# Kernel optimization log

Measured on AMD Instinct MI355X. Metric: run time of the kernel, lower is better.

Reference implementation:

```python
import jax, jax.numpy as jnp
import numpy as np

D_MODEL = 1024
NUM_HEADS = 16
D_K = D_MODEL // NUM_HEADS


def setup_inputs() -> dict:
    key = jax.random.key(0)
    ks = jax.random.split(key, 9)
    B, S = 2, 2048
    s_in = 1.0 / np.sqrt(D_MODEL)
    x = jax.random.normal(ks[0], (B, S, D_MODEL), dtype=jnp.float32)
    # Linear weights stored as (in_features, out_features): y = x @ W + b
    Wq = jax.random.uniform(ks[1], (D_MODEL, D_MODEL), jnp.float32, -s_in, s_in)
    bq = jax.random.uniform(ks[2], (D_MODEL,), jnp.float32, -s_in, s_in)
    Wk = jax.random.uniform(ks[3], (D_MODEL, D_K), jnp.float32, -s_in, s_in)
    bk = jax.random.uniform(ks[4], (D_K,), jnp.float32, -s_in, s_in)
    Wv = jax.random.uniform(ks[5], (D_MODEL, D_K), jnp.float32, -s_in, s_in)
    bv = jax.random.uniform(ks[6], (D_K,), jnp.float32, -s_in, s_in)
    Wo = jax.random.uniform(ks[7], (D_MODEL, D_MODEL), jnp.float32, -s_in, s_in)
    bo = jax.random.uniform(ks[8], (D_MODEL,), jnp.float32, -s_in, s_in)
    return {"x": x, "Wq": Wq, "bq": bq, "Wk": Wk, "bk": bk,
            "Wv": Wv, "bv": bv, "Wo": Wo, "bo": bo}


def reference(x, Wq, bq, Wk, bk, Wv, bv, Wo, bo):
    B, S, _ = x.shape
    H, Dk = NUM_HEADS, D_K
    # Projections
    Q = (x @ Wq + bq).reshape(B, S, H, Dk).transpose(0, 2, 1, 3)  # [B,H,S,Dk]
    K = x @ Wk + bk                                               # [B,S,Dk] single KV head
    V = x @ Wv + bv                                               # [B,S,Dk]
    # Scores: query heads broadcast against the single shared KV head
    scores = jnp.einsum('bhqd,bkd->bhqk', Q, K) / jnp.sqrt(jnp.float32(Dk))
    attn = jax.nn.softmax(scores, axis=-1)                        # [B,H,S,S]
    out = jnp.einsum('bhqk,bkd->bhqd', attn, V)                   # [B,H,S,Dk]
    out = out.transpose(0, 2, 1, 3).reshape(B, S, H * Dk)         # [B,S,d_model]
    return out @ Wo + bo
```

## Files before the change

### kernel.cpp

```cpp
#include <hip/hip_runtime.h>
#include <hip/hip_bf16.h>

typedef __attribute__((ext_vector_type(8))) short bf16x8;
typedef __attribute__((ext_vector_type(4))) float f32x4;
typedef __attribute__((ext_vector_type(16))) float f32x16;
typedef __attribute__((ext_vector_type(4))) unsigned short ushort4v;

#define QSCALE 0.1803368801111204f

__device__ __forceinline__ unsigned short f2bf(float f) {
  union { float f; unsigned int u; } x; x.f = f;
  unsigned int u = x.u;
  unsigned int r = (u + 0x7fffu + ((u >> 16) & 1u)) >> 16;
  return (unsigned short)r;
}

__device__ __forceinline__ void gll16(const unsigned short* g, unsigned short* l) {
  __builtin_amdgcn_global_load_lds(
      (const __attribute__((address_space(1))) unsigned int*)g,
      (__attribute__((address_space(3))) unsigned int*)l, 16, 0, 0);
}

__global__ __launch_bounds__(256) void prep_kernel(
    const float* __restrict__ x,
    const float* __restrict__ Wq, const float* __restrict__ Wk,
    const float* __restrict__ Wv, const float* __restrict__ Wo,
    unsigned short* __restrict__ xb,
    unsigned short* __restrict__ QKVt, unsigned short* __restrict__ Wot) {
  int z = blockIdx.z;
  if (z == 4) {
    size_t base = ((size_t)(blockIdx.y * 32 + blockIdx.x)) * 4096 + threadIdx.x * 16;
#pragma unroll
    for (int c = 0; c < 4; ++c) {
      float4 v = *(const float4*)(x + base + c * 4);
      ushort4v o = { f2bf(v.x), f2bf(v.y), f2bf(v.z), f2bf(v.w) };
      *(ushort4v*)(xb + base + c * 4) = o;
    }
    return;
  }
  __shared__ float t[32][33];
  const float* src;
  unsigned short* dst;
  int C, rowoff;
  if (z == 0)      { src = Wq; dst = QKVt; C = 1024; rowoff = 0; }
  else if (z == 1) { src = Wk; dst = QKVt; C = 64;   rowoff = 1024; }
  else if (z == 2) { src = Wv; dst = QKVt; C = 64;   rowoff = 1088; }
  else             { src = Wo; dst = Wot;  C = 1024; rowoff = 0; }
  int c0 = blockIdx.x * 32, r0 = blockIdx.y * 32;
  if (c0 >= C) return;
  int tx = threadIdx.x & 31, ty = threadIdx.x >> 5;
#pragma unroll
  for (int i = 0; i < 32; i += 8)
    t[ty + i][tx] = src[(size_t)(r0 + ty + i) * C + c0 + tx];
  __syncthreads();
#pragma unroll
  for (int i = 0; i < 32; i += 8)
    dst[(size_t)(rowoff + c0 + ty + i) * 1024 + r0 + tx] = f2bf(t[tx][ty + i]);
}

template <typename OutT, bool QKVMODE>
__global__ __launch_bounds__(512, 2) void gemm_bf16_kernel(
    const unsigned short* __restrict__ A, const unsigned short* __restrict__ Bt,
    const float* __restrict__ b0, const float* __restrict__ b1,
    const float* __restrict__ b2, OutT* __restrict__ C,
    unsigned short* __restrict__ Vt, int M, int N, int K) {
  __shared__ __align__(16) unsigned short As[2][128 * 32];
  __shared__ __align__(16) unsigned short Bs[2][64 * 32];
  int tid = threadIdx.x;
  int wid = tid >> 6, lane = tid & 63;
  int l15 = lane & 15, quad = lane >> 4;
  int m0 = blockIdx.x * 128, n0 = blockIdx.y * 64;
  int mw = (wid >> 1) * 32, nw = (wid & 1) * 32;
  f32x4 acc[2][2];
#pragma unroll
  for (int i = 0; i < 2; i++)
#pragma unroll
    for (int j = 0; j < 2; j++)
#pragma unroll
      for (int e = 0; e < 4; ++e) acc[i][j][e] = 0.f;

  bool isA = (wid < 4);
  int u = tid & 255;
  int srow = u >> 2;
  int gq = (u & 3) ^ ((srow >> 1) & 3);
  const unsigned short* Ag = A + (size_t)(m0 + srow) * K + gq * 8;
  const unsigned short* Bg = Bt + (size_t)(n0 + srow) * K + gq * 8;

  if (isA) {
    gll16(Ag, As[0] + u * 8);
    gll16(Ag + (size_t)64 * K, As[0] + 2048 + u * 8);
  } else {
    gll16(Bg, Bs[0] + u * 8);
  }

  for (int k0 = 0; k0 < K; k0 += 32) {
    int cur = (k0 >> 5) & 1;
    if (k0 + 32 < K) {
      int nxt = cur ^ 1;
      if (isA) {
        gll16(Ag + k0 + 32, As[nxt] + u * 8);
        gll16(Ag + (size_t)64 * K + k0 + 32, As[nxt] + 2048 + u * 8);
        asm volatile("s_waitcnt vmcnt(2)" ::: "memory");
      } else {
        gll16(Bg + k0 + 32, Bs[nxt] + u * 8);
        asm volatile("s_waitcnt vmcnt(1)" ::: "memory");
      }
    } else {
      asm volatile("s_waitcnt vmcnt(0)" ::: "memory");
    }
    __builtin_amdgcn_s_barrier();
    __builtin_amdgcn_sched_barrier(0);
    const unsigned short* Asb = As[cur];
    const unsigned short* Bsb = Bs[cur];
    bf16x8 af[2], bfr[2];
#pragma unroll
    for (int t = 0; t < 2; ++t) {
      int row = mw + t * 16 + l15;
      af[t] = *(const bf16x8*)(Asb + row * 32 + ((quad ^ ((row >> 1) & 3)) * 8));
    }
#pragma unroll
    for (int t = 0; t < 2; ++t) {
      int row = nw + t * 16 + l15;
      bfr[t] = *(const bf16x8*)(Bsb + row * 32 + ((quad ^ ((row >> 1) & 3)) * 8));
    }
#pragma unroll
    for (int mt = 0; mt < 2; ++mt)
#pragma unroll
      for (int nt = 0; nt < 2; ++nt)
        acc[mt][nt] = __builtin_amdgcn_mfma_f32_16x16x32_bf16(
            af[mt], bfr[nt], acc[mt][nt], 0, 0, 0);
    asm volatile("s_waitcnt lgkmcnt(0)" ::: "memory");
    __builtin_amdgcn_sched_barrier(0);
    __builtin_amdgcn_s_barrier();
  }
#pragma unroll
  for (int mt = 0; mt < 2; ++mt)
#pragma unroll
    for (int nt = 0; nt < 2; ++nt) {
      int col = n0 + nw + nt * 16 + l15;
      float bias, cs;
      if constexpr (QKVMODE) {
        bias = (col < 1024) ? b0[col] : ((col < 1088) ? b1[col - 1024] : b2[col - 1088]);
        cs = (col < 1024) ? QSCALE : 1.0f;
      } else {
        bias = b0[col];
        cs = 1.0f;
      }
#pragma unroll
      for (int r = 0; r < 4; ++r) {
        int row = m0 + mw + mt * 16 + quad * 4 + r;
        float v = (acc[mt][nt][r] + bias) * cs;
        if constexpr (sizeof(OutT) == 2)
          C[(size_t)row * N + col] = f2bf(v);
        else
          C[(size_t)row * N + col] = v;
        if constexpr (QKVMODE) {
          if (col >= 1088)
            Vt[((size_t)(row >> 11) * 64 + (col - 1088)) * 2048 + (row & 2047)] =
                f2bf(v);
        }
      }
    }
}

__global__ __launch_bounds__(512, 4) void flash_attn_kernel(
    const unsigned short* __restrict__ QKV,
    const unsigned short* __restrict__ Vt,
    unsigned short* __restrict__ AO) {
  constexpr int S = 2048, LDQ = 1152;
  constexpr int PK = 72;
  __shared__ __align__(16) unsigned short smem[2][2][64 * PK];
  int tid = threadIdx.x;
  int wid = tid >> 6, lane = tid & 63;
  int l31 = lane & 31, half = lane >> 5;
  int p = wid & 3, ks = wid >> 2;
  int q0 = blockIdx.x * 128, h = blockIdx.y, b = blockIdx.z;

  const unsigned short* Qb =
      QKV + (size_t)(b * S + q0 + p * 32 + l31) * LDQ + h * 64 + half * 8;
  bf16x8 qf[4];
#pragma unroll
  for (int f = 0; f < 4; ++f) qf[f] = *(const bf16x8*)(Qb + f * 16);

  int u = tid & 255, sl = tid >> 8;
  int srow = u >> 2, sc = (u & 3) * 8;
  const unsigned short* Kgb = QKV + ((size_t)b * S) * LDQ + 1024;
  const unsigned short* Vgb = Vt + ((size_t)(b * 64 + srow)) * 2048;

  f32x16 oa0, oa1;
#pragma unroll
  for (int r = 0; r < 16; ++r) { oa0[r] = 0.f; oa1[r] = 0.f; }
  float rs = 0.f;

  int kb0 = sl * 1024;
  bf16x8 ka = *(const bf16x8*)(Kgb + (size_t)(kb0 + srow) * LDQ + sc);
  bf16x8 kc = *(const bf16x8*)(Kgb + (size_t)(kb0 + srow) * LDQ + sc + 32);
  bf16x8 va = *(const bf16x8*)(Vgb + kb0 + sc);
  bf16x8 vc = *(const bf16x8*)(Vgb + kb0 + sc + 32);

  unsigned short* Ksb = smem[ks][0];
  unsigned short* Vsb = smem[ks][1];

  for (int kt = 0; kt < 16; ++kt) {
    *(bf16x8*)(smem[sl][0] + srow * PK + sc) = ka;
    *(bf16x8*)(smem[sl][0] + srow * PK + sc + 32) = kc;
    *(bf16x8*)(smem[sl][1] + srow * PK + sc) = va;
    *(bf16x8*)(smem[sl][1] + srow * PK + sc + 32) = vc;
    __syncthreads();
    if (kt + 1 < 16) {
      int kbn = sl * 1024 + (kt + 1) * 64;
      ka = *(const bf16x8*)(Kgb + (size_t)(kbn + srow) * LDQ + sc);
      kc = *(const bf16x8*)(Kgb + (size_t)(kbn + srow) * LDQ + sc + 32);
      va = *(const bf16x8*)(Vgb + kbn + sc);
      vc = *(const bf16x8*)(Vgb + kbn + sc + 32);
    }

#pragma unroll
    for (int n2 = 0; n2 < 2; ++n2) {
      f32x16 sacc;
#pragma unroll
      for (int i = 0; i < 16; ++i) sacc[i] = 0.f;
#pragma unroll
      for (int s = 0; s < 4; ++s) {
        bf16x8 kf =
            *(const bf16x8*)(Ksb + (n2 * 32 + l31) * PK + s * 16 + half * 8);
        sacc = __builtin_amdgcn_mfma_f32_32x32x16_bf16(kf, qf[s], sacc, 0, 0, 0);
      }
#pragma unroll
      for (int t = 0; t < 2; ++t) {
        float pr[8];
#pragma unroll
        for (int j = 0; j < 8; ++j) {
          pr[j] = __builtin_amdgcn_exp2f(sacc[t * 8 + j]);
          rs += pr[j];
        }
        unsigned w0A, w1A, w0B, w1B;
        asm("v_cvt_pk_bf16_f32 %0, %1, %2" : "=v"(w0A) : "v"(pr[0]), "v"(pr[1]));
        asm("v_cvt_pk_bf16_f32 %0, %1, %2" : "=v"(w1A) : "v"(pr[2]), "v"(pr[3]));
        asm("v_cvt_pk_bf16_f32 %0, %1, %2" : "=v"(w0B) : "v"(pr[4]), "v"(pr[5]));
        asm("v_cvt_pk_bf16_f32 %0, %1, %2" : "=v"(w1B) : "v"(pr[6]), "v"(pr[7]));
        asm volatile("v_permlane32_swap_b32 %0, %1" : "+v"(w0A), "+v"(w0B));
        asm volatile("v_permlane32_swap_b32 %0, %1" : "+v"(w1A), "+v"(w1B));
        union { unsigned u[4]; bf16x8 v; } afu;
        afu.u[0] = w0A; afu.u[1] = w1A; afu.u[2] = w0B; afu.u[3] = w1B;
        int sg = n2 * 2 + t;
        bf16x8 vf0 = *(const bf16x8*)(Vsb + (l31) * PK + sg * 16 + half * 8);
        bf16x8 vf1 = *(const bf16x8*)(Vsb + (32 + l31) * PK + sg * 16 + half * 8);
        oa0 = __builtin_amdgcn_mfma_f32_32x32x16_bf16(afu.v, vf0, oa0, 0, 0, 0);
        oa1 = __builtin_amdgcn_mfma_f32_32x32x16_bf16(afu.v, vf1, oa1, 0, 0, 0);
      }
    }
    __syncthreads();
  }

  float rsf = rs + __shfl_xor(rs, 32, 64);

  float* Cb = (float*)smem;
  if (ks == 1) {
#pragma unroll
    for (int r = 0; r < 16; ++r) {
      int row = (r & 3) + 8 * (r >> 2) + 4 * half;
      Cb[(p * 32 + row) * 66 + l31] = oa0[r];
      Cb[(p * 32 + row) * 66 + 32 + l31] = oa1[r];
    }
    if (half == 0) Cb[(p * 32 + l31) * 66 + 64] = rsf;
  } else {
    if (half == 0) Cb[(p * 32 + l31) * 66 + 65] = rsf;
  }
  __syncthreads();
  if (ks == 0) {
    unsigned short* Ob = AO + (size_t)(b * S + q0 + p * 32) * 1024 + h * 64;
#pragma unroll
    for (int r = 0; r < 16; ++r) {
      int row = (r & 3) + 8 * (r >> 2) + 4 * half;
      float p0 = Cb[(p * 32 + row) * 66 + l31];
      float p1 = Cb[(p * 32 + row) * 66 + 32 + l31];
      float inv = 1.0f / (Cb[(p * 32 + row) * 66 + 64] + Cb[(p * 32 + row) * 66 + 65]);
      Ob[(size_t)row * 1024 + l31] = f2bf((oa0[r] + p0) * inv);
      Ob[(size_t)row * 1024 + 32 + l31] = f2bf((oa1[r] + p1) * inv);
    }
  }
}

extern "C" void kernel_launch(void* const* d_in, const int* in_sizes, int n_in,
                              void* d_out, int out_size, void* d_ws, size_t ws_size,
                              hipStream_t stream) {
  const float* x  = (const float*)d_in[0];
  const float* Wq = (const float*)d_in[1];
  const float* bq = (const float*)d_in[2];
  const float* Wk = (const float*)d_in[3];
  const float* bk = (const float*)d_in[4];
  const float* Wv = (const float*)d_in[5];
  const float* bv = (const float*)d_in[6];
  const float* Wo = (const float*)d_in[7];
  const float* bo = (const float*)d_in[8];
  float* out = (float*)d_out;

  constexpr int B = 2, S = 2048, D = 1024, Dk = 64, H = 16;
  constexpr int M = B * S;
  constexpr int NQKV = D + 2 * Dk;

  char* ws = (char*)d_ws;
  unsigned short* xb   = (unsigned short*)ws; ws += (size_t)M * D * 2;
  unsigned short* QKVt = (unsigned short*)ws; ws += (size_t)NQKV * D * 2;
  unsigned short* Wot  = (unsigned short*)ws; ws += (size_t)D * D * 2;
  unsigned short* QKV  = (unsigned short*)ws; ws += (size_t)M * NQKV * 2;
  unsigned short* Vtb  = (unsigned short*)ws; ws += (size_t)B * Dk * S * 2;
  unsigned short* AO   = (unsigned short*)ws; ws += (size_t)M * D * 2;

  prep_kernel<<<dim3(32, 32, 5), 256, 0, stream>>>(x, Wq, Wk, Wv, Wo, xb, QKVt, Wot);

  gemm_bf16_kernel<unsigned short, true><<<dim3(M / 128, NQKV / 64), 512, 0, stream>>>(
      xb, QKVt, bq, bk, bv, QKV, Vtb, M, NQKV, D);

  flash_attn_kernel<<<dim3(S / 128, H, B), 512, 0, stream>>>(QKV, Vtb, AO);

  gemm_bf16_kernel<float, false><<<dim3(M / 128, D / 64), 512, 0, stream>>>(
      AO, Wot, bo, nullptr, nullptr, out, nullptr, M, D, D);
}
```

Baseline: 168.3 us.

## Load K/V fragments directly from global in attention, drop LDS staging

The flash attention kernel no longer stages K and V tiles through shared memory with per-tile barriers. Each wave reads its K and transposed-V MFMA fragments straight from global memory, relying on L2 and L1 caching since the single KV head is shared across all query heads. Blocks shrink to 256 threads and 64 queries, and the grid doubles. This removes the LDS writes and syncthreads in the main loop, at the cost of strided uncoalesced global loads, especially on V rows 4 KB apart, and no explicit prefetch.

```diff
diff --git a/kernel.cpp b/kernel.cpp
--- a/kernel.cpp
+++ b/kernel.cpp
@@ -163,18 +163,17 @@
     }
 }
 
-__global__ __launch_bounds__(512, 4) void flash_attn_kernel(
+__global__ __launch_bounds__(256, 4) void flash_attn_kernel(
     const unsigned short* __restrict__ QKV,
     const unsigned short* __restrict__ Vt,
     unsigned short* __restrict__ AO) {
   constexpr int S = 2048, LDQ = 1152;
-  constexpr int PK = 72;
-  __shared__ __align__(16) unsigned short smem[2][2][64 * PK];
+  __shared__ float Cb[2 * 32 * 66];
   int tid = threadIdx.x;
   int wid = tid >> 6, lane = tid & 63;
   int l31 = lane & 31, half = lane >> 5;
-  int p = wid & 3, ks = wid >> 2;
-  int q0 = blockIdx.x * 128, h = blockIdx.y, b = blockIdx.z;
+  int p = wid & 1, ks = wid >> 1;
+  int q0 = blockIdx.x * 64, h = blockIdx.y, b = blockIdx.z;
 
   const unsigned short* Qb =
       QKV + (size_t)(b * S + q0 + p * 32 + l31) * LDQ + h * 64 + half * 8;
@@ -182,50 +181,32 @@
 #pragma unroll
   for (int f = 0; f < 4; ++f) qf[f] = *(const bf16x8*)(Qb + f * 16);
 
-  int u = tid & 255, sl = tid >> 8;
-  int srow = u >> 2, sc = (u & 3) * 8;
-  const unsigned short* Kgb = QKV + ((size_t)b * S) * LDQ + 1024;
-  const unsigned short* Vgb = Vt + ((size_t)(b * 64 + srow)) * 2048;
+  const unsigned short* Kg = QKV + (size_t)(b * S + ks * 1024) * LDQ + 1024;
+  const unsigned short* Vg = Vt + (size_t)(b * 64) * 2048 + ks * 1024;
 
   f32x16 oa0, oa1;
 #pragma unroll
   for (int r = 0; r < 16; ++r) { oa0[r] = 0.f; oa1[r] = 0.f; }
   float rs = 0.f;
 
-  int kb0 = sl * 1024;
-  bf16x8 ka = *(const bf16x8*)(Kgb + (size_t)(kb0 + srow) * LDQ + sc);
-  bf16x8 kc = *(const bf16x8*)(Kgb + (size_t)(kb0 + srow) * LDQ + sc + 32);
-  bf16x8 va = *(const bf16x8*)(Vgb + kb0 + sc);
-  bf16x8 vc = *(const bf16x8*)(Vgb + kb0 + sc + 32);
-
-  unsigned short* Ksb = smem[ks][0];
-  unsigned short* Vsb = smem[ks][1];
-
+#pragma unroll 1
   for (int kt = 0; kt < 16; ++kt) {
-    *(bf16x8*)(smem[sl][0] + srow * PK + sc) = ka;
-    *(bf16x8*)(smem[sl][0] + srow * PK + sc + 32) = kc;
-    *(bf16x8*)(smem[sl][1] + srow * PK + sc) = va;
-    *(bf16x8*)(smem[sl][1] + srow * PK + sc + 32) = vc;
-    __syncthreads();
-    if (kt + 1 < 16) {
-      int kbn = sl * 1024 + (kt + 1) * 64;
-      ka = *(const bf16x8*)(Kgb + (size_t)(kbn + srow) * LDQ + sc);
-      kc = *(const bf16x8*)(Kgb + (size_t)(kbn + srow) * LDQ + sc + 32);
-      va = *(const bf16x8*)(Vgb + kbn + sc);
-      vc = *(const bf16x8*)(Vgb + kbn + sc + 32);
-    }
-
+    int kb = kt * 64;
 #pragma unroll
     for (int n2 = 0; n2 < 2; ++n2) {
+      const unsigned short* Kr =
+          Kg + (size_t)(kb + n2 * 32 + l31) * LDQ + half * 8;
+      bf16x8 kf0 = *(const bf16x8*)(Kr);
+      bf16x8 kf1 = *(const bf16x8*)(Kr + 16);
+      bf16x8 kf2 = *(const bf16x8*)(Kr + 32);
+      bf16x8 kf3 = *(const bf16x8*)(Kr + 48);
       f32x16 sacc;
 #pragma unroll
       for (int i = 0; i < 16; ++i) sacc[i] = 0.f;
-#pragma unroll
-      for (int s = 0; s < 4; ++s) {
-        bf16x8 kf =
-            *(const bf16x8*)(Ksb + (n2 * 32 + l31) * PK + s * 16 + half * 8);
-        sacc = __builtin_amdgcn_mfma_f32_32x32x16_bf16(kf, qf[s], sacc, 0, 0, 0);
-      }
+      sacc = __builtin_amdgcn_mfma_f32_32x32x16_bf16(kf0, qf[0], sacc, 0, 0, 0);
+      sacc = __builtin_amdgcn_mfma_f32_32x32x16_bf16(kf1, qf[1], sacc, 0, 0, 0);
+      sacc = __builtin_amdgcn_mfma_f32_32x32x16_bf16(kf2, qf[2], sacc, 0, 0, 0);
+      sacc = __builtin_amdgcn_mfma_f32_32x32x16_bf16(kf3, qf[3], sacc, 0, 0, 0);
 #pragma unroll
       for (int t = 0; t < 2; ++t) {
         float pr[8];
@@ -244,18 +225,17 @@
         union { unsigned u[4]; bf16x8 v; } afu;
         afu.u[0] = w0A; afu.u[1] = w1A; afu.u[2] = w0B; afu.u[3] = w1B;
         int sg = n2 * 2 + t;
-        bf16x8 vf0 = *(const bf16x8*)(Vsb + (l31) * PK + sg * 16 + half * 8);
-        bf16x8 vf1 = *(const bf16x8*)(Vsb + (32 + l31) * PK + sg * 16 + half * 8);
+        const unsigned short* Vr = Vg + kb + sg * 16 + half * 8;
+        bf16x8 vf0 = *(const bf16x8*)(Vr + (size_t)l31 * 2048);
+        bf16x8 vf1 = *(const bf16x8*)(Vr + (size_t)(32 + l31) * 2048);
         oa0 = __builtin_amdgcn_mfma_f32_32x32x16_bf16(afu.v, vf0, oa0, 0, 0, 0);
         oa1 = __builtin_amdgcn_mfma_f32_32x32x16_bf16(afu.v, vf1, oa1, 0, 0, 0);
       }
     }
-    __syncthreads();
   }
 
   float rsf = rs + __shfl_xor(rs, 32, 64);
 
-  float* Cb = (float*)smem;
   if (ks == 1) {
 #pragma unroll
     for (int r = 0; r < 16; ++r) {
@@ -275,7 +255,8 @@
       int row = (r & 3) + 8 * (r >> 2) + 4 * half;
       float p0 = Cb[(p * 32 + row) * 66 + l31];
       float p1 = Cb[(p * 32 + row) * 66 + 32 + l31];
-      float inv = 1.0f / (Cb[(p * 32 + row) * 66 + 64] + Cb[(p * 32 + row) * 66 + 65]);
+      float inv =
+          1.0f / (Cb[(p * 32 + row) * 66 + 64] + Cb[(p * 32 + row) * 66 + 65]);
       Ob[(size_t)row * 1024 + l31] = f2bf((oa0[r] + p0) * inv);
       Ob[(size_t)row * 1024 + 32 + l31] = f2bf((oa1[r] + p1) * inv);
     }
@@ -313,7 +294,7 @@
   gemm_bf16_kernel<unsigned short, true><<<dim3(M / 128, NQKV / 64), 512, 0, stream>>>(
       xb, QKVt, bq, bk, bv, QKV, Vtb, M, NQKV, D);
 
-  flash_attn_kernel<<<dim3(S / 128, H, B), 512, 0, stream>>>(QKV, Vtb, AO);
+  flash_attn_kernel<<<dim3(S / 64, H, B), 256, 0, stream>>>(QKV, Vtb, AO);
 
   gemm_bf16_kernel<float, false><<<dim3(M / 128, D / 64), 512, 0, stream>>>(
       AO, Wot, bo, nullptr, nullptr, out, nullptr, M, D, D);
```

Result: slower. 249.5 us (+48.2%).
